# Optimization experiments

Measured on AMD Instinct MI355X. Metric: run time of the kernel, lower is better.

## Reference

```python
import jax, jax.numpy as jnp
import numpy as np

N, D_IN, D_OUT = 8192, 768, 64

def setup_inputs() -> dict:
    key = jax.random.key(0)
    k1, k2, k3, k4 = jax.random.split(key, 4)
    x = jax.random.normal(k1, (N, D_IN), dtype=jnp.float32)
    # nn.Linear weight is [d_out, d_in]; we store transposed [d_in, d_out] for x @ W
    s = 1.0 / np.sqrt(D_IN)
    Wk = jax.random.normal(k2, (D_IN, D_OUT), dtype=jnp.float32) * s
    Wq = jax.random.normal(k3, (D_IN, D_OUT), dtype=jnp.float32) * s
    Wv = jax.random.normal(k4, (D_IN, D_OUT), dtype=jnp.float32) * s
    return {"x": x, "Wk": Wk, "Wq": Wq, "Wv": Wv}

def reference(x, Wk, Wq, Wv):
    inv_sqrt_dk = 1.0 / np.sqrt(D_OUT)
    # Faithful to source: k_w output used as the left matrix, q_w output as right
    wq = x @ Wk            # [N, d_out]  (source: weighted_q = k_w(x))
    wk = x @ Wq            # [N, d_out]  (source: weighted_k = q_w(x))
    scores = wq @ wk.T     # [N, N]
    attn = jax.nn.softmax(scores * inv_sqrt_dk, axis=-1)
    wv = x @ Wv            # [N, d_out]
    return attn @ wv       # [N, d_out]
```

## Files before the change

kernel.cpp:

```cpp
#include <hip/hip_runtime.h>
#include <hip/hip_bf16.h>

#define NTOK 8192
#define DIN  768

typedef float  f32x4  __attribute__((ext_vector_type(4)));
typedef float  f32x16 __attribute__((ext_vector_type(16)));
typedef short  bf16x8 __attribute__((ext_vector_type(8)));

static __device__ __forceinline__ unsigned short f2bf(float f) {
  unsigned int u = __float_as_uint(f);
  u += 0x7FFFu + ((u >> 16) & 1u);
  return (unsigned short)(u >> 16);
}
static __device__ __forceinline__ unsigned cvt_pk(float lo, float hi) {
  unsigned r;
  asm("v_cvt_pk_bf16_f32 %0, %1, %2" : "=v"(r) : "v"(lo), "v"(hi));
  return r;
}
static __device__ __forceinline__ void pswap(unsigned &x, unsigned &y) {
  auto r = __builtin_amdgcn_permlane32_swap(x, y, false, false);
  x = r[0]; y = r[1];
}

union U4 { unsigned u[4]; bf16x8 v; uint4 q; };

__global__ __launch_bounds__(256) void prep_wf(
    const float* __restrict__ Wk, const float* __restrict__ Wq,
    const float* __restrict__ Wv, unsigned short* __restrict__ Wf) {
  int tid  = blockIdx.x * 256 + threadIdx.x;
  int lane = tid & 63;
  int chunk = tid >> 6;
  int g = chunk / 24, kt = chunk - g * 24;
  int col = (g & 3) * 16 + (lane & 15);
  int k0  = kt * 32 + ((lane >> 4) & 3) * 8;
  int ws  = g >> 2;
  const float* W = (ws == 0) ? Wk : (ws == 1) ? Wq : Wv;
  U4 o;
#pragma unroll
  for (int jj = 0; jj < 4; ++jj)
    o.u[jj] = cvt_pk(W[(k0 + 2 * jj) * 64 + col], W[(k0 + 2 * jj + 1) * 64 + col]);
  *(uint4*)(Wf + (size_t)tid * 8) = o.q;
}

__global__ __launch_bounds__(768) void proj_qkv(
    const float* __restrict__ x, const unsigned short* __restrict__ Wf,
    unsigned short* __restrict__ Qb, unsigned short* __restrict__ Kf,
    unsigned short* __restrict__ Vf) {
  __shared__ uint4 xl4[16 * 96];
  int tid = threadIdx.x;
  int rowBase = blockIdx.x * 16;

#pragma unroll
  for (int s = 0; s < 2; ++s) {
    int idx = s * 768 + tid;
    int row = idx / 96, b = idx - row * 96;
    const float4* xp = (const float4*)(x + (size_t)(rowBase + row) * DIN + b * 8);
    float4 v0 = xp[0], v1 = xp[1];
    U4 o;
    o.u[0] = cvt_pk(v0.x, v0.y); o.u[1] = cvt_pk(v0.z, v0.w);
    o.u[2] = cvt_pk(v1.x, v1.y); o.u[3] = cvt_pk(v1.z, v1.w);
    xl4[row * 96 + (b ^ (row & 7))] = o.q;
  }
  __syncthreads();

  int wv = tid >> 6, lane = tid & 63;
  int r = lane & 15, hi = lane >> 4;

  f32x4 acc = (f32x4){0.f, 0.f, 0.f, 0.f};
  const bf16x8* xfr = (const bf16x8*)xl4;
#pragma unroll 4
  for (int kt = 0; kt < 24; ++kt) {
    bf16x8 af = xfr[r * 96 + ((kt * 4 + hi) ^ (r & 7))];
    bf16x8 wf = *(const bf16x8*)(Wf + ((size_t)(wv * 24 + kt) * 64 + lane) * 8);
    acc = __builtin_amdgcn_mfma_f32_16x16x32_bf16(af, wf, acc, 0, 0, 0);
  }

  int g  = wv;
  int W  = g >> 2;
  int cc = (g & 3) * 16 + r;
  if (W == 0) {
#pragma unroll
    for (int i = 0; i < 4; ++i)
      Qb[(rowBase + hi * 4 + i) * 64 + cc] = f2bf(acc[i] * 0.18033688f);
  } else if (W == 1) {
    int cbit = cc >> 4, hb = (cc >> 3) & 1, j = cc & 7;
#pragma unroll
    for (int i = 0; i < 4; ++i) {
      int grow = rowBase + hi * 4 + i;
      Kf[(((size_t)(grow >> 5) * 4 + cbit) * 64 + (grow & 31) + 32 * hb) * 8 + j] =
          f2bf(acc[i]);
    }
  } else {
    int grow0 = rowBase + hi * 4;
    int T  = grow0 >> 5, ks = (grow0 >> 4) & 1;
    int dh = cc >> 5;
    int hb = (hi >> 1) & 1, j0 = (hi & 1) * 4;
    size_t addr = (((size_t)T * 4 + dh * 2 + ks) * 64 + (cc & 31) + 32 * hb) * 8 + j0;
    uint2 pk = {cvt_pk(acc[0], acc[1]), cvt_pk(acc[2], acc[3])};
    *(uint2*)(Vf + addr) = pk;
  }
}

__global__ __launch_bounds__(512, 2) void attn_kernel(
    const unsigned short* __restrict__ Qb, const unsigned short* __restrict__ Kf,
    const unsigned short* __restrict__ Vf, float* __restrict__ Pnum,
    float* __restrict__ Pden) {
  int bid  = blockIdx.x;
  int kb   = bid & 7;
  int qt   = bid >> 3;
  int wv   = threadIdx.x >> 6;
  int lane = threadIdx.x & 63;
  int l31 = lane & 31, hi = lane >> 5;
  int q0g  = qt * 256 + wv * 32;

  bf16x8 qf[4];
#pragma unroll
  for (int c = 0; c < 4; ++c)
    qf[c] = *(const bf16x8*)(Qb + (size_t)(q0g + l31) * 64 + c * 16 + hi * 8);

  f32x16 acc0, acc1, zz;
#pragma unroll
  for (int i = 0; i < 16; ++i) { acc0[i] = 0.f; acc1[i] = 0.f; zz[i] = 0.f; }
  float rsum = 0.f;

  const unsigned short* kf_l = Kf + (size_t)(kb * 32) * 2048 + (size_t)lane * 8;
  const unsigned short* vf_l = Vf + (size_t)(kb * 32) * 2048 + (size_t)lane * 8;

#pragma unroll 2
  for (int t = 0; t < 32; ++t) {
    const unsigned short* kc = kf_l + (size_t)t * 2048;
    bf16x8 kf0 = *(const bf16x8*)(kc);
    bf16x8 kf1 = *(const bf16x8*)(kc + 512);
    bf16x8 kf2 = *(const bf16x8*)(kc + 1024);
    bf16x8 kf3 = *(const bf16x8*)(kc + 1536);
    const unsigned short* vc = vf_l + (size_t)t * 2048;
    bf16x8 vf00 = *(const bf16x8*)(vc);
    bf16x8 vf01 = *(const bf16x8*)(vc + 512);
    bf16x8 vf10 = *(const bf16x8*)(vc + 1024);
    bf16x8 vf11 = *(const bf16x8*)(vc + 1536);

    f32x16 s;
    s = __builtin_amdgcn_mfma_f32_32x32x16_bf16(kf0, qf[0], zz, 0, 0, 0);
    s = __builtin_amdgcn_mfma_f32_32x32x16_bf16(kf1, qf[1], s, 0, 0, 0);
    s = __builtin_amdgcn_mfma_f32_32x32x16_bf16(kf2, qf[2], s, 0, 0, 0);
    s = __builtin_amdgcn_mfma_f32_32x32x16_bf16(kf3, qf[3], s, 0, 0, 0);

    float p[16];
#pragma unroll
    for (int i = 0; i < 16; ++i) {
      p[i] = __builtin_amdgcn_exp2f(s[i] - 17.3123405f);
      rsum += p[i];
    }

    unsigned a0 = cvt_pk(p[0], p[1]),   b0 = cvt_pk(p[4], p[5]);
    pswap(a0, b0);
    unsigned c0 = cvt_pk(p[2], p[3]),   d0 = cvt_pk(p[6], p[7]);
    pswap(c0, d0);
    unsigned a1 = cvt_pk(p[8], p[9]),   b1 = cvt_pk(p[12], p[13]);
    pswap(a1, b1);
    unsigned c1 = cvt_pk(p[10], p[11]), d1 = cvt_pk(p[14], p[15]);
    pswap(c1, d1);
    U4 pa0, pa1;
    pa0.u[0] = a0; pa0.u[1] = c0; pa0.u[2] = b0; pa0.u[3] = d0;
    pa1.u[0] = a1; pa1.u[1] = c1; pa1.u[2] = b1; pa1.u[3] = d1;

    acc0 = __builtin_amdgcn_mfma_f32_32x32x16_bf16(pa0.v, vf00, acc0, 0, 0, 0);
    acc1 = __builtin_amdgcn_mfma_f32_32x32x16_bf16(pa0.v, vf10, acc1, 0, 0, 0);
    acc0 = __builtin_amdgcn_mfma_f32_32x32x16_bf16(pa1.v, vf01, acc0, 0, 0, 0);
    acc1 = __builtin_amdgcn_mfma_f32_32x32x16_bf16(pa1.v, vf11, acc1, 0, 0, 0);
  }

#pragma unroll
  for (int rg = 0; rg < 16; ++rg) {
    int qr = (rg & 3) + 8 * (rg >> 2) + 4 * hi;
    size_t base = ((size_t)kb * NTOK + q0g + qr) * 64;
    Pnum[base + l31]      = acc0[rg];
    Pnum[base + 32 + l31] = acc1[rg];
  }
  float rtot = rsum + __shfl_xor(rsum, 32);
  if (hi == 0) Pden[(size_t)kb * NTOK + q0g + l31] = rtot;
}

__global__ __launch_bounds__(256) void reduce_out(
    const float* __restrict__ Pnum, const float* __restrict__ Pden,
    float* __restrict__ out) {
  int gid = blockIdx.x * 256 + threadIdx.x;
  int q  = gid >> 4;
  int c4 = (gid & 15) * 4;
  float4 n = {0.f, 0.f, 0.f, 0.f};
  float den = 0.f;
#pragma unroll
  for (int p = 0; p < 8; ++p) {
    float4 o = *(const float4*)(Pnum + ((size_t)p * NTOK + q) * 64 + c4);
    n.x += o.x; n.y += o.y; n.z += o.z; n.w += o.w;
    den += Pden[(size_t)p * NTOK + q];
  }
  float inv = 1.f / den;
  float4 res = {n.x * inv, n.y * inv, n.z * inv, n.w * inv};
  *(float4*)(out + (size_t)q * 64 + c4) = res;
}

extern "C" void kernel_launch(void* const* d_in, const int* in_sizes, int n_in,
                              void* d_out, int out_size, void* d_ws, size_t ws_size,
                              hipStream_t stream) {
  const float* x  = (const float*)d_in[0];
  const float* Wk = (const float*)d_in[1];
  const float* Wq = (const float*)d_in[2];
  const float* Wv = (const float*)d_in[3];

  unsigned short* Qb = (unsigned short*)d_ws;
  unsigned short* Kf = Qb + (size_t)NTOK * 64;
  unsigned short* Vf = Kf + (size_t)NTOK * 64;
  unsigned short* Wf = Vf + (size_t)NTOK * 64;
  float* Pnum = (float*)((char*)d_ws + (8u << 20));
  float* Pden = (float*)((char*)d_ws + (40u << 20));

  prep_wf<<<72, 256, 0, stream>>>(Wk, Wq, Wv, Wf);
  proj_qkv<<<NTOK / 16, 768, 0, stream>>>(x, Wf, Qb, Kf, Vf);
  attn_kernel<<<256, 512, 0, stream>>>(Qb, Kf, Vf, Pnum, Pden);
  reduce_out<<<512, 256, 0, stream>>>(Pnum, Pden, (float*)d_out);
}
```

Measured before the change: 109.9 us.

## Split keys 16 ways, double-buffer K fragments, prioritize MFMA issue

Result: slower. 112.2 us (+2.1%).

```diff
diff --git a/kernel.cpp b/kernel.cpp
--- a/kernel.cpp
+++ b/kernel.cpp
@@ -102,13 +102,58 @@
   }
 }
 
-__global__ __launch_bounds__(512, 2) void attn_kernel(
+#define ATTN_TILE(K0, K1, K2, K3, N0, N1, N2, N3, t, nt)                      \
+  {                                                                           \
+    f32x16 s;                                                                 \
+    _Pragma("unroll") for (int i = 0; i < 16; ++i) s[i] = 0.f;                \
+    __builtin_amdgcn_s_setprio(1);                                            \
+    s = __builtin_amdgcn_mfma_f32_32x32x16_bf16(K0, qf[0], s, 0, 0, 0);       \
+    s = __builtin_amdgcn_mfma_f32_32x32x16_bf16(K1, qf[1], s, 0, 0, 0);       \
+    s = __builtin_amdgcn_mfma_f32_32x32x16_bf16(K2, qf[2], s, 0, 0, 0);       \
+    s = __builtin_amdgcn_mfma_f32_32x32x16_bf16(K3, qf[3], s, 0, 0, 0);       \
+    __builtin_amdgcn_s_setprio(0);                                            \
+    const unsigned short* kc_ = kf_l + (size_t)(nt) * 2048;                   \
+    N0 = *(const bf16x8*)(kc_);        N1 = *(const bf16x8*)(kc_ + 512);      \
+    N2 = *(const bf16x8*)(kc_ + 1024); N3 = *(const bf16x8*)(kc_ + 1536);     \
+    const unsigned short* vc_ = vf_l + (size_t)(t) * 2048;                    \
+    bf16x8 V0 = *(const bf16x8*)(vc_);                                        \
+    bf16x8 V1 = *(const bf16x8*)(vc_ + 512);                                  \
+    bf16x8 V2 = *(const bf16x8*)(vc_ + 1024);                                 \
+    bf16x8 V3 = *(const bf16x8*)(vc_ + 1536);                                 \
+    float p[16];                                                              \
+    _Pragma("unroll") for (int i = 0; i < 16; i += 4) {                       \
+      p[i]     = __builtin_amdgcn_exp2f(s[i]     - 17.3123405f);              \
+      p[i + 1] = __builtin_amdgcn_exp2f(s[i + 1] - 17.3123405f);              \
+      p[i + 2] = __builtin_amdgcn_exp2f(s[i + 2] - 17.3123405f);              \
+      p[i + 3] = __builtin_amdgcn_exp2f(s[i + 3] - 17.3123405f);              \
+      r0 += p[i]; r1 += p[i + 1]; r2 += p[i + 2]; r3 += p[i + 3];             \
+    }                                                                         \
+    unsigned a0 = cvt_pk(p[0], p[1]),   b0 = cvt_pk(p[4], p[5]);              \
+    pswap(a0, b0);                                                            \
+    unsigned c0 = cvt_pk(p[2], p[3]),   d0 = cvt_pk(p[6], p[7]);              \
+    pswap(c0, d0);                                                            \
+    unsigned a1 = cvt_pk(p[8], p[9]),   b1 = cvt_pk(p[12], p[13]);            \
+    pswap(a1, b1);                                                            \
+    unsigned c1 = cvt_pk(p[10], p[11]), d1 = cvt_pk(p[14], p[15]);            \
+    pswap(c1, d1);                                                            \
+    U4 pa0, pa1;                                                              \
+    pa0.u[0] = a0; pa0.u[1] = c0; pa0.u[2] = b0; pa0.u[3] = d0;               \
+    pa1.u[0] = a1; pa1.u[1] = c1; pa1.u[2] = b1; pa1.u[3] = d1;               \
+    __builtin_amdgcn_s_setprio(1);                                            \
+    acc0 = __builtin_amdgcn_mfma_f32_32x32x16_bf16(pa0.v, V0, acc0, 0, 0, 0); \
+    acc1 = __builtin_amdgcn_mfma_f32_32x32x16_bf16(pa0.v, V2, acc1, 0, 0, 0); \
+    acc0 = __builtin_amdgcn_mfma_f32_32x32x16_bf16(pa1.v, V1, acc0, 0, 0, 0); \
+    acc1 = __builtin_amdgcn_mfma_f32_32x32x16_bf16(pa1.v, V3, acc1, 0, 0, 0); \
+    __builtin_amdgcn_s_setprio(0);                                            \
+  }
+
+__global__ __launch_bounds__(512, 4) void attn_kernel(
     const unsigned short* __restrict__ Qb, const unsigned short* __restrict__ Kf,
     const unsigned short* __restrict__ Vf, float* __restrict__ Pnum,
     float* __restrict__ Pden) {
   int bid  = blockIdx.x;
-  int kb   = bid & 7;
-  int qt   = bid >> 3;
+  int kb   = bid & 15;
+  int qt   = bid >> 4;
   int wv   = threadIdx.x >> 6;
   int lane = threadIdx.x & 63;
   int l31 = lane & 31, hi = lane >> 5;
@@ -119,56 +164,23 @@
   for (int c = 0; c < 4; ++c)
     qf[c] = *(const bf16x8*)(Qb + (size_t)(q0g + l31) * 64 + c * 16 + hi * 8);
 
-  f32x16 acc0, acc1, zz;
-#pragma unroll
-  for (int i = 0; i < 16; ++i) { acc0[i] = 0.f; acc1[i] = 0.f; zz[i] = 0.f; }
-  float rsum = 0.f;
-
-  const unsigned short* kf_l = Kf + (size_t)(kb * 32) * 2048 + (size_t)lane * 8;
-  const unsigned short* vf_l = Vf + (size_t)(kb * 32) * 2048 + (size_t)lane * 8;
-
-#pragma unroll 2
-  for (int t = 0; t < 32; ++t) {
-    const unsigned short* kc = kf_l + (size_t)t * 2048;
-    bf16x8 kf0 = *(const bf16x8*)(kc);
-    bf16x8 kf1 = *(const bf16x8*)(kc + 512);
-    bf16x8 kf2 = *(const bf16x8*)(kc + 1024);
-    bf16x8 kf3 = *(const bf16x8*)(kc + 1536);
-    const unsigned short* vc = vf_l + (size_t)t * 2048;
-    bf16x8 vf00 = *(const bf16x8*)(vc);
-    bf16x8 vf01 = *(const bf16x8*)(vc + 512);
-    bf16x8 vf10 = *(const bf16x8*)(vc + 1024);
-    bf16x8 vf11 = *(const bf16x8*)(vc + 1536);
-
-    f32x16 s;
-    s = __builtin_amdgcn_mfma_f32_32x32x16_bf16(kf0, qf[0], zz, 0, 0, 0);
-    s = __builtin_amdgcn_mfma_f32_32x32x16_bf16(kf1, qf[1], s, 0, 0, 0);
-    s = __builtin_amdgcn_mfma_f32_32x32x16_bf16(kf2, qf[2], s, 0, 0, 0);
-    s = __builtin_amdgcn_mfma_f32_32x32x16_bf16(kf3, qf[3], s, 0, 0, 0);
-
-    float p[16];
-#pragma unroll
-    for (int i = 0; i < 16; ++i) {
-      p[i] = __builtin_amdgcn_exp2f(s[i] - 17.3123405f);
-      rsum += p[i];
-    }
-
-    unsigned a0 = cvt_pk(p[0], p[1]),   b0 = cvt_pk(p[4], p[5]);
-    pswap(a0, b0);
-    unsigned c0 = cvt_pk(p[2], p[3]),   d0 = cvt_pk(p[6], p[7]);
-    pswap(c0, d0);
-    unsigned a1 = cvt_pk(p[8], p[9]),   b1 = cvt_pk(p[12], p[13]);
-    pswap(a1, b1);
-    unsigned c1 = cvt_pk(p[10], p[11]), d1 = cvt_pk(p[14], p[15]);
-    pswap(c1, d1);
-    U4 pa0, pa1;
-    pa0.u[0] = a0; pa0.u[1] = c0; pa0.u[2] = b0; pa0.u[3] = d0;
-    pa1.u[0] = a1; pa1.u[1] = c1; pa1.u[2] = b1; pa1.u[3] = d1;
-
-    acc0 = __builtin_amdgcn_mfma_f32_32x32x16_bf16(pa0.v, vf00, acc0, 0, 0, 0);
-    acc1 = __builtin_amdgcn_mfma_f32_32x32x16_bf16(pa0.v, vf10, acc1, 0, 0, 0);
-    acc0 = __builtin_amdgcn_mfma_f32_32x32x16_bf16(pa1.v, vf01, acc0, 0, 0, 0);
-    acc1 = __builtin_amdgcn_mfma_f32_32x32x16_bf16(pa1.v, vf11, acc1, 0, 0, 0);
+  f32x16 acc0, acc1;
+#pragma unroll
+  for (int i = 0; i < 16; ++i) { acc0[i] = 0.f; acc1[i] = 0.f; }
+  float r0 = 0.f, r1 = 0.f, r2 = 0.f, r3 = 0.f;
+
+  const unsigned short* kf_l = Kf + (size_t)(kb << 4) * 2048 + (size_t)lane * 8;
+  const unsigned short* vf_l = Vf + (size_t)(kb << 4) * 2048 + (size_t)lane * 8;
+
+  bf16x8 kA0, kA1, kA2, kA3, kB0, kB1, kB2, kB3;
+  kA0 = *(const bf16x8*)(kf_l);
+  kA1 = *(const bf16x8*)(kf_l + 512);
+  kA2 = *(const bf16x8*)(kf_l + 1024);
+  kA3 = *(const bf16x8*)(kf_l + 1536);
+
+  for (int t = 0; t < 16; t += 2) {
+    ATTN_TILE(kA0, kA1, kA2, kA3, kB0, kB1, kB2, kB3, t, t + 1);
+    ATTN_TILE(kB0, kB1, kB2, kB3, kA0, kA1, kA2, kA3, t + 1, (t + 2) & 15);
   }
 
 #pragma unroll
@@ -178,6 +190,7 @@
     Pnum[base + l31]      = acc0[rg];
     Pnum[base + 32 + l31] = acc1[rg];
   }
+  float rsum = (r0 + r1) + (r2 + r3);
   float rtot = rsum + __shfl_xor(rsum, 32);
   if (hi == 0) Pden[(size_t)kb * NTOK + q0g + l31] = rtot;
 }
@@ -191,7 +204,7 @@
   float4 n = {0.f, 0.f, 0.f, 0.f};
   float den = 0.f;
 #pragma unroll
-  for (int p = 0; p < 8; ++p) {
+  for (int p = 0; p < 16; ++p) {
     float4 o = *(const float4*)(Pnum + ((size_t)p * NTOK + q) * 64 + c4);
     n.x += o.x; n.y += o.y; n.z += o.z; n.w += o.w;
     den += Pden[(size_t)p * NTOK + q];
@@ -218,6 +231,6 @@
 
   prep_wf<<<72, 256, 0, stream>>>(Wk, Wq, Wv, Wf);
   proj_qkv<<<NTOK / 16, 768, 0, stream>>>(x, Wf, Qb, Kf, Vf);
-  attn_kernel<<<256, 512, 0, stream>>>(Qb, Kf, Vf, Pnum, Pden);
+  attn_kernel<<<512, 512, 0, stream>>>(Qb, Kf, Vf, Pnum, Pden);
   reduce_out<<<512, 256, 0, stream>>>(Pnum, Pden, (float*)d_out);
 }
```
